# Kernel optimization log

Hardware: AMD Instinct MI355X
Metric: run time of the kernel (lower is better)

Reference implementation:

```python
import jax, jax.numpy as jnp
import numpy as np

N_NODES = 50000
N_EDGES = 1000000
D = 66
NEG_SLOPE = 0.2
EPS_BN = 1e-5


def _glorot(key, shape):
    fan = sum(shape)
    lim = jnp.sqrt(6.0 / fan)
    return jax.random.uniform(key, shape, jnp.float32, -lim, lim)


def setup_inputs() -> dict:
    key = jax.random.key(0)
    ks = jax.random.split(key, 40)
    inp = {
        'h': jax.random.normal(ks[0], (N_NODES, D), jnp.float32),
        'edge_index': jax.random.randint(ks[1], (2, N_EDGES), 0, N_NODES, jnp.int32),
        'edge_weight': jax.random.uniform(ks[2], (N_EDGES, 1), jnp.float32),
        'bn_gamma': jnp.ones((D,), jnp.float32),
        'bn_beta': jnp.zeros((D,), jnp.float32),
    }
    i = 3
    for l in (1, 2, 3):
        inp[f'W{l}'] = _glorot(ks[i], (D, D)); i += 1
        inp[f'b{l}'] = jnp.zeros((D,), jnp.float32)
        inp[f'att_src{l}'] = _glorot(ks[i], (D,)); i += 1
        inp[f'att_dst{l}'] = _glorot(ks[i], (D,)); i += 1
        inp[f'We{l}'] = _glorot(ks[i], (1, D)); i += 1
        inp[f'att_e{l}'] = _glorot(ks[i], (D,)); i += 1
    dims = [(D, D), (D, D), (D, D), (D, D), (D, 22)]
    for l, (din, dout) in enumerate(dims, start=1):
        inp[f'fc{l}_w'] = _glorot(ks[i], (din, dout)); i += 1
        inp[f'fc{l}_b'] = jnp.zeros((dout,), jnp.float32)
    return inp


def _gat_conv(h, src, dst, edge_weight, W, b, att_src, att_dst, We, att_e):
    x = h @ W                                     # [N, D]
    a_src = x @ att_src                           # [N]
    a_dst = x @ att_dst                           # [N]
    a_e = (edge_weight @ We) @ att_e              # [E]
    alpha = a_src[src] + a_dst[dst] + a_e         # [E]
    alpha = jnp.where(alpha > 0, alpha, NEG_SLOPE * alpha)
    # scatter-softmax over destination nodes
    m = jax.ops.segment_max(alpha, dst, num_segments=N_NODES)
    m = jnp.where(jnp.isfinite(m), m, 0.0)
    ex = jnp.exp(alpha - m[dst])
    denom = jax.ops.segment_sum(ex, dst, num_segments=N_NODES)
    coef = ex / (denom[dst] + 1e-16)              # [E]
    out = jax.ops.segment_sum(coef[:, None] * x[src], dst, num_segments=N_NODES)
    return out + b


def reference(h, edge_index, edge_weight, bn_gamma, bn_beta,
              W1, b1, att_src1, att_dst1, We1, att_e1,
              W2, b2, att_src2, att_dst2, We2, att_e2,
              W3, b3, att_src3, att_dst3, We3, att_e3,
              fc1_w, fc1_b, fc2_w, fc2_b, fc3_w, fc3_b,
              fc4_w, fc4_b, fc5_w, fc5_b):
    src, dst = edge_index[0], edge_index[1]
    # BatchNorm1d (training-mode batch statistics, biased variance)
    mean = h.mean(0)
    var = ((h - mean) ** 2).mean(0)
    x = (h - mean) * jax.lax.rsqrt(var + EPS_BN) * bn_gamma + bn_beta
    x = jax.nn.relu(_gat_conv(x, src, dst, edge_weight, W1, b1, att_src1, att_dst1, We1, att_e1))
    x = jax.nn.relu(_gat_conv(x, src, dst, edge_weight, W2, b2, att_src2, att_dst2, We2, att_e2))
    x = jax.nn.relu(_gat_conv(x, src, dst, edge_weight, W3, b3, att_src3, att_dst3, We3, att_e3))
    x = jax.nn.relu(x @ fc1_w + fc1_b)
    x = jax.nn.relu(x @ fc2_w + fc2_b)
    x = jax.nn.relu(x @ fc3_w + fc3_b)
    x = jax.nn.relu(x @ fc4_w + fc4_b)
    return x @ fc5_w + fc5_b
```

## Files before the change

kernel.cpp:

```cpp
#include <hip/hip_runtime.h>
#include <math.h>

#define D 66
#define SP 68
#define NEG_SLOPE 0.2f
#define CAP 6144

typedef short s8v __attribute__((ext_vector_type(8)));
typedef float f4v __attribute__((ext_vector_type(4)));

__device__ __forceinline__ float lrelu(float a){ return a > 0.f ? a : NEG_SLOPE * a; }
__device__ __forceinline__ void fma4(float4& a, float s, const float4& w){
  a.x = fmaf(s, w.x, a.x); a.y = fmaf(s, w.y, a.y);
  a.z = fmaf(s, w.z, a.z); a.w = fmaf(s, w.w, a.w);
}
__device__ __forceinline__ unsigned short bf16r(float f){
  unsigned u = __float_as_uint(f);
  u += 0x7FFFu + ((u >> 16) & 1u);
  return (unsigned short)(u >> 16);
}
__device__ __forceinline__ float bf16f(unsigned short b){
  return __uint_as_float(((unsigned)b) << 16);
}
__device__ __forceinline__ void split8t(const float* p, s8v& a0, s8v& a1, s8v& a2){
  #pragma unroll
  for (int j = 0; j < 8; j++){
    float v = p[j];
    unsigned u0 = __float_as_uint(v) & 0xFFFF0000u;
    float r1 = v - __uint_as_float(u0);
    unsigned u1 = __float_as_uint(r1) & 0xFFFF0000u;
    float r2 = r1 - __uint_as_float(u1);
    unsigned u2 = __float_as_uint(r2);
    a0[j] = (short)(u0 >> 16);
    a1[j] = (short)(u1 >> 16);
    a2[j] = (short)(u2 >> 16);
  }
}
#define MM6(acc, a0, a1, a2, b0v, b1v, b2v)                                \
  acc = __builtin_amdgcn_mfma_f32_16x16x32_bf16(a0, b0v, acc, 0, 0, 0);    \
  acc = __builtin_amdgcn_mfma_f32_16x16x32_bf16(a1, b0v, acc, 0, 0, 0);    \
  acc = __builtin_amdgcn_mfma_f32_16x16x32_bf16(a0, b1v, acc, 0, 0, 0);    \
  acc = __builtin_amdgcn_mfma_f32_16x16x32_bf16(a2, b0v, acc, 0, 0, 0);    \
  acc = __builtin_amdgcn_mfma_f32_16x16x32_bf16(a1, b1v, acc, 0, 0, 0);    \
  acc = __builtin_amdgcn_mfma_f32_16x16x32_bf16(a0, b2v, acc, 0, 0, 0);

__global__ __launch_bounds__(256) void k_stats_hist(const float* __restrict__ h, const int* __restrict__ dst,
                                                    float* __restrict__ sums, int* __restrict__ bhist,
                                                    int n, int E){
  int t = threadIdx.x;
  if (blockIdx.x < 256){
    __shared__ float ls[2 * D];
    if (t < 2 * D) ls[t] = 0.f;
    __syncthreads();
    int rpb = (n + 255) / 256;
    int r0 = blockIdx.x * rpb;
    int r1 = min(n, r0 + rpb);
    if (t < 3 * D){
      int c = t % D, seg = t / D;
      float s1 = 0.f, s2 = 0.f;
      for (int r = r0 + seg; r < r1; r += 3){
        float v = h[(size_t)r * D + c];
        s1 += v; s2 += v * v;
      }
      atomicAdd(&ls[c], s1);
      atomicAdd(&ls[D + c], s2);
    }
    __syncthreads();
    if (t < 2 * D) atomicAdd(&sums[t], ls[t]);
  } else {
    __shared__ int hh[256];
    hh[t] = 0;
    __syncthreads();
    int stride = 256 * 256;
    for (int e = (blockIdx.x - 256) * 256 + t; e < E; e += stride)
      atomicAdd(&hh[dst[e] >> 8], 1);
    __syncthreads();
    if (hh[t]) atomicAdd(&bhist[t], hh[t]);
  }
}

struct PrepArgs {
  const float *sums, *gamma, *beta;
  const float *We[3], *ae[3];
  const float *gw[3];
  const float *fw[5], *fb[5];
  float *misc; short *W0, *W1, *W2; short *F0, *F1, *F2; float *bpack;
  int n;
};

__global__ __launch_bounds__(256) void k_prep(PrepArgs pa){
  int t = threadIdx.x;
  if (blockIdx.x == 0){
    if (t < D){
      float mean = pa.sums[t] / (float)pa.n;
      float var  = pa.sums[D + t] / (float)pa.n - mean * mean;
      float inv  = rsqrtf(var + 1e-5f);
      float sc = pa.gamma[t] * inv;
      pa.misc[t] = sc;
      pa.misc[D + t] = pa.beta[t] - mean * sc;
    } else if (t >= D && t < D + 3){
      int l = t - D;
      float c = 0.f;
      for (int d = 0; d < D; d++) c += pa.We[l][d] * pa.ae[l][d];
      pa.misc[2 * D + l] = c;
    }
  } else if (blockIdx.x <= 12){
    int tid = (blockIdx.x - 1) * 256 + t;
    if (tid >= 3 * 960) return;
    int L = tid & 63;
    int ct = (tid >> 6) % 15;
    int lay = tid / 960;
    const float* w = pa.gw[lay];
    int c = ct / 5, tt = ct % 5;
    int nn = tt * 16 + (L & 15);
    int kb = c * 32 + (L >> 4) * 8;
    #pragma unroll
    for (int j = 0; j < 8; j++){
      int k = kb + j;
      float v = (k < D && nn < D) ? w[k * D + nn] : 0.f;
      unsigned short b0 = bf16r(v);  float f0 = bf16f(b0);
      float r1 = v - f0;
      unsigned short b1 = bf16r(r1); float f1 = bf16f(b1);
      unsigned short b2 = bf16r(r1 - f1);
      pa.W0[tid * 8 + j] = (short)b0;
      pa.W1[tid * 8 + j] = (short)b1;
      pa.W2[tid * 8 + j] = (short)b2;
    }
  } else {
    int tid = (blockIdx.x - 13) * 256 + t;
    if (tid < 5 * 960){
      int L = tid & 63;
      int ct = (tid >> 6) % 15;
      int lay = tid / 960;
      const float* w = pa.fw[lay];
      int ncol = (lay == 4) ? 22 : D;
      int c = ct / 5, tt = ct % 5;
      int nn = tt * 16 + (L & 15);
      int kb = c * 32 + (L >> 4) * 8;
      #pragma unroll
      for (int j = 0; j < 8; j++){
        int k = kb + j;
        float v = (k < D && nn < ncol) ? w[k * ncol + nn] : 0.f;
        unsigned short b0 = bf16r(v);  float f0 = bf16f(b0);
        float r1 = v - f0;
        unsigned short b1 = bf16r(r1); float f1 = bf16f(b1);
        unsigned short b2 = bf16r(r1 - f1);
        pa.F0[tid * 8 + j] = (short)b0;
        pa.F1[tid * 8 + j] = (short)b1;
        pa.F2[tid * 8 + j] = (short)b2;
      }
    } else if (tid < 5 * 960 + 400){
      int i = tid - 5 * 960;
      int lay = i / 80, col = i % 80;
      int ncol = (lay == 4) ? 22 : D;
      pa.bpack[i] = (col < ncol) ? pa.fb[lay][col] : 0.f;
    }
  }
}

__global__ void k_bscan(const int* __restrict__ bhist, int* __restrict__ bbase,
                        int* __restrict__ gcur, int* __restrict__ rowptr, int N, int E){
  __shared__ int sh[256];
  int t = threadIdx.x;
  int v = bhist[t];
  sh[t] = v; __syncthreads();
  for (int o = 1; o < 256; o <<= 1){
    int u = (t >= o) ? sh[t - o] : 0;
    __syncthreads();
    sh[t] += u;
    __syncthreads();
  }
  int ex = sh[t] - v;
  bbase[t] = ex;
  gcur[t] = ex;
  if (t == 255){ bbase[256] = sh[255]; rowptr[N] = E; }
}

#define PCHUNK 4096
__global__ __launch_bounds__(256) void k_part(const int* __restrict__ src, const int* __restrict__ dst,
                                              const float* __restrict__ ew,
                                              int* __restrict__ gcur, int2* __restrict__ tmp, int E){
  __shared__ int hist[256];
  __shared__ int base[256];
  int t = threadIdx.x;
  int e0 = blockIdx.x * PCHUNK;
  int eend = min(E, e0 + PCHUNK);
  hist[t] = 0;
  __syncthreads();
  for (int e = e0 + t; e < eend; e += 256)
    atomicAdd(&hist[dst[e] >> 8], 1);
  __syncthreads();
  if (hist[t] > 0) base[t] = atomicAdd(&gcur[t], hist[t]);
  hist[t] = 0;
  __syncthreads();
  for (int e = e0 + t; e < eend; e += 256){
    int d = dst[e];
    int b = d >> 8;
    int off = atomicAdd(&hist[b], 1);
    tmp[base[b] + off] = make_int2((src[e] & 0xffff) | ((d & 255) << 16), __float_as_int(ew[e]));
  }
}

__global__ __launch_bounds__(256) void k_bsort(const int2* __restrict__ tmp, const int* __restrict__ bbase,
                                               int2* __restrict__ epair, int* __restrict__ rowptr, int N){
  __shared__ int2 ebuf[CAP];
  __shared__ int lcnt[256];
  __shared__ int sc[256];
  __shared__ int lcur[256];
  int b = blockIdx.x, t = threadIdx.x;
  int s0 = bbase[b], s1 = bbase[b + 1];
  int cnt = s1 - s0;
  lcnt[t] = 0;
  __syncthreads();
  for (int j = t; j < cnt; j += 256){
    int2 e = tmp[s0 + j];
    if (j < CAP) ebuf[j] = e;
    atomicAdd(&lcnt[(e.x >> 16) & 255], 1);
  }
  __syncthreads();
  int v = lcnt[t];
  sc[t] = v; __syncthreads();
  for (int o = 1; o < 256; o <<= 1){
    int u = (t >= o) ? sc[t - o] : 0;
    __syncthreads();
    sc[t] += u;
    __syncthreads();
  }
  int ex = sc[t] - v;
  int node = (b << 8) + t;
  if (node < N) rowptr[node] = s0 + ex;
  lcur[t] = ex;
  __syncthreads();
  for (int j = t; j < cnt; j += 256){
    int2 e = (j < CAP) ? ebuf[j] : tmp[s0 + j];
    int i = (e.x >> 16) & 255;
    int p = atomicAdd(&lcur[i], 1);
    epair[s0 + p] = make_int2(e.x & 0xffff, e.y);
  }
}

template<bool BN_IN>
__global__ __launch_bounds__(256) void k_mm(const float* __restrict__ X,
    const short* __restrict__ W0, const short* __restrict__ W1, const short* __restrict__ W2,
    const float* __restrict__ att_s, const float* __restrict__ att_d,
    const float* __restrict__ bn,
    float* __restrict__ Y, float* __restrict__ a_src, float* __restrict__ a_dst, int n){
  const int wv = threadIdx.x >> 6, L = threadIdx.x & 63;
  const int quad = L >> 4, m = L & 15;
  const int row0 = blockIdx.x * 64 + wv * 16;
  const int lrow = min(row0 + m, n - 1);
  f4v acc[5];
  #pragma unroll
  for (int t = 0; t < 5; t++) acc[t] = (f4v){0.f,0.f,0.f,0.f};

  #pragma unroll
  for (int c = 0; c < 3; c++){
    float xv[8];
    if (c < 2){
      if (BN_IN){
        const float* hr = X + (size_t)lrow * D + c * 32 + quad * 8;
        #pragma unroll
        for (int j = 0; j < 8; j += 2){
          float2 hv = *(const float2*)(hr + j);
          int col = c * 32 + quad * 8 + j;
          xv[j]     = hv.x * bn[col]     + bn[D + col];
          xv[j + 1] = hv.y * bn[col + 1] + bn[D + col + 1];
        }
      } else {
        const float* xr = X + (size_t)lrow * SP;
        float4 p0 = *(const float4*)&xr[c * 32 + quad * 8];
        float4 p1 = *(const float4*)&xr[c * 32 + quad * 8 + 4];
        xv[0] = p0.x; xv[1] = p0.y; xv[2] = p0.z; xv[3] = p0.w;
        xv[4] = p1.x; xv[5] = p1.y; xv[6] = p1.z; xv[7] = p1.w;
      }
    } else {
      #pragma unroll
      for (int j = 0; j < 8; j++) xv[j] = 0.f;
      if (quad == 0){
        if (BN_IN){
          float2 hv = *(const float2*)(X + (size_t)lrow * D + 64);
          xv[0] = hv.x * bn[64] + bn[D + 64];
          xv[1] = hv.y * bn[65] + bn[D + 65];
        } else {
          float4 p0 = *(const float4*)&X[(size_t)lrow * SP + 64];
          xv[0] = p0.x; xv[1] = p0.y; xv[2] = p0.z; xv[3] = p0.w;
        }
      }
    }
    s8v a0, a1, a2;
    split8t(xv, a0, a1, a2);
    const short* b0p = W0 + (c * 5) * 512 + L * 8;
    const short* b1p = W1 + (c * 5) * 512 + L * 8;
    const short* b2p = W2 + (c * 5) * 512 + L * 8;
    #pragma unroll
    for (int t = 0; t < 5; t++){
      s8v b0v = *(const s8v*)(b0p + t * 512);
      s8v b1v = *(const s8v*)(b1p + t * 512);
      s8v b2v = *(const s8v*)(b2p + t * 512);
      MM6(acc[t], a0, a1, a2, b0v, b1v, b2v)
    }
  }

  float ps[4] = {0.f,0.f,0.f,0.f}, pd[4] = {0.f,0.f,0.f,0.f};
  #pragma unroll
  for (int t = 0; t < 5; t++){
    int col = t * 16 + m;
    float as_v = 0.f, ad_v = 0.f;
    if (col < D){ as_v = att_s[col]; ad_v = att_d[col]; }
    #pragma unroll
    for (int r = 0; r < 4; r++){
      ps[r] += acc[t][r] * as_v;
      pd[r] += acc[t][r] * ad_v;
    }
  }
  #pragma unroll
  for (int r = 0; r < 4; r++){
    int rw = row0 + quad * 4 + r;
    if (rw < n){
      float* yr = Y + (size_t)rw * SP;
      #pragma unroll
      for (int t = 0; t < 4; t++) yr[t * 16 + m] = acc[t][r];
      if (m < 4) yr[64 + m] = (m < 2) ? acc[4][r] : 0.f;
    }
  }
  #pragma unroll
  for (int o = 1; o <= 8; o <<= 1){
    #pragma unroll
    for (int r = 0; r < 4; r++){
      ps[r] += __shfl_xor(ps[r], o);
      pd[r] += __shfl_xor(pd[r], o);
    }
  }
  if (m == 0){
    #pragma unroll
    for (int r = 0; r < 4; r++){
      int rw = row0 + quad * 4 + r;
      if (rw < n){ a_src[rw] = ps[r]; a_dst[rw] = pd[r]; }
    }
  }
}

#define FST 84
__global__ __launch_bounds__(256) void k_fcmm(const float* __restrict__ X,
    const short* __restrict__ W0, const short* __restrict__ W1, const short* __restrict__ W2,
    const float* __restrict__ bpack, float* __restrict__ out, int n){
  __shared__ __align__(16) float xs[4][16][FST];
  const int wv = threadIdx.x >> 6, L = threadIdx.x & 63;
  const int quad = L >> 4, m = L & 15;
  const int row0 = blockIdx.x * 64 + wv * 16;
  const int lrow = min(row0 + m, n - 1);
  const float* xr = X + (size_t)lrow * SP;

  for (int l = 0; l < 5; l++){
    const int NTl = (l == 4) ? 2 : 5;
    f4v acc[5];
    #pragma unroll
    for (int t = 0; t < 5; t++) acc[t] = (f4v){0.f,0.f,0.f,0.f};
    #pragma unroll
    for (int c = 0; c < 3; c++){
      float xv[8];
      if (l == 0){
        if (c < 2){
          float4 p0 = *(const float4*)&xr[c * 32 + quad * 8];
          float4 p1 = *(const float4*)&xr[c * 32 + quad * 8 + 4];
          xv[0] = p0.x; xv[1] = p0.y; xv[2] = p0.z; xv[3] = p0.w;
          xv[4] = p1.x; xv[5] = p1.y; xv[6] = p1.z; xv[7] = p1.w;
        } else {
          float4 p0 = make_float4(0.f, 0.f, 0.f, 0.f);
          if (quad == 0) p0 = *(const float4*)&xr[64];
          xv[0] = p0.x; xv[1] = p0.y; xv[2] = p0.z; xv[3] = p0.w;
          xv[4] = 0.f; xv[5] = 0.f; xv[6] = 0.f; xv[7] = 0.f;
        }
      } else {
        if (c == 2 && quad >= 2){
          #pragma unroll
          for (int j = 0; j < 8; j++) xv[j] = 0.f;
        } else {
          float4 p0 = *(const float4*)&xs[wv][m][c * 32 + quad * 8];
          float4 p1 = *(const float4*)&xs[wv][m][c * 32 + quad * 8 + 4];
          xv[0] = p0.x; xv[1] = p0.y; xv[2] = p0.z; xv[3] = p0.w;
          xv[4] = p1.x; xv[5] = p1.y; xv[6] = p1.z; xv[7] = p1.w;
        }
      }
      s8v a0, a1, a2;
      split8t(xv, a0, a1, a2);
      const short* b0p = W0 + ((l * 3 + c) * 5) * 512 + L * 8;
      const short* b1p = W1 + ((l * 3 + c) * 5) * 512 + L * 8;
      const short* b2p = W2 + ((l * 3 + c) * 5) * 512 + L * 8;
      for (int t = 0; t < NTl; t++){
        s8v b0v = *(const s8v*)(b0p + t * 512);
        s8v b1v = *(const s8v*)(b1p + t * 512);
        s8v b2v = *(const s8v*)(b2p + t * 512);
        MM6(acc[t], a0, a1, a2, b0v, b1v, b2v)
      }
    }
    if (l < 4){
      #pragma unroll
      for (int t = 0; t < 5; t++){
        int col = t * 16 + m;
        float bv = bpack[l * 80 + col];
        #pragma unroll
        for (int r = 0; r < 4; r++){
          float v = acc[t][r] + bv;
          xs[wv][quad * 4 + r][col] = v > 0.f ? v : 0.f;
        }
      }
      __asm__ volatile("" ::: "memory");
    } else {
      #pragma unroll
      for (int t = 0; t < 2; t++){
        int col = t * 16 + m;
        #pragma unroll
        for (int r = 0; r < 4; r++){
          int rw = row0 + quad * 4 + r;
          if (col < 22 && rw < n) out[(size_t)rw * 22 + col] = acc[t][r] + bpack[4 * 80 + col];
        }
      }
    }
  }
}

__global__ __launch_bounds__(256) void k_agg(const float* __restrict__ y,
                                             const float* __restrict__ a_src, const float* __restrict__ a_dst,
                                             const int* __restrict__ rowptr, const int2* __restrict__ epair,
                                             const float* __restrict__ misc, int cidx,
                                             const float* __restrict__ bias,
                                             float* __restrict__ xout, int n){
  const int wid  = (int)((blockIdx.x * (size_t)blockDim.x + threadIdx.x) >> 6);
  const int lane = threadIdx.x & 63;
  if (wid >= n) return;
  const int beg = rowptr[wid];
  const int deg = rowptr[wid + 1] - beg;
  const float ce  = misc[2 * D + cidx];
  const float adn = a_dst[wid];
  const int g = lane >> 3, q = lane & 7;

  float4 accA = make_float4(0.f,0.f,0.f,0.f);
  float4 accB = make_float4(0.f,0.f,0.f,0.f);
  float2 tacc = make_float2(0.f,0.f);

  if (deg <= 64){
    int s = 0; float al = -INFINITY;
    bool act = lane < deg;
    if (act){
      int2 ep = epair[beg + lane];
      s = ep.x;
      al = lrelu(a_src[s] + adn + ce * __int_as_float(ep.y));
    }
    float mx = al;
    #pragma unroll
    for (int o = 32; o; o >>= 1) mx = fmaxf(mx, __shfl_xor(mx, o));
    float ex = act ? __expf(al - mx) : 0.f;
    float sum = ex;
    #pragma unroll
    for (int o = 32; o; o >>= 1) sum += __shfl_xor(sum, o);
    float coef = ex * (1.f / (sum + 1e-16f));
    for (int e0 = 0; e0 < deg; e0 += 8){
      int e = e0 + g;
      int   st = __shfl(s, e);
      float ct = __shfl(coef, e);
      if (e < deg){
        const float* row = y + (size_t)st * SP;
        float4 y0 = *(const float4*)&row[4 * q];
        float4 y1 = *(const float4*)&row[32 + 4 * q];
        fma4(accA, ct, y0);
        fma4(accB, ct, y1);
        if (q == 0){
          float2 tv = *(const float2*)&row[64];
          tacc.x += ct * tv.x; tacc.y += ct * tv.y;
        }
      }
    }
  } else {
    float mx = -INFINITY;
    for (int j0 = 0; j0 < deg; j0 += 64){
      int j = j0 + lane;
      if (j < deg){
        int2 ep = epair[beg + j];
        mx = fmaxf(mx, lrelu(a_src[ep.x] + adn + ce * __int_as_float(ep.y)));
      }
    }
    #pragma unroll
    for (int o = 32; o; o >>= 1) mx = fmaxf(mx, __shfl_xor(mx, o));
    float sum = 0.f;
    for (int j0 = 0; j0 < deg; j0 += 64){
      int j = j0 + lane;
      if (j < deg){
        int2 ep = epair[beg + j];
        sum += __expf(lrelu(a_src[ep.x] + adn + ce * __int_as_float(ep.y)) - mx);
      }
    }
    #pragma unroll
    for (int o = 32; o; o >>= 1) sum += __shfl_xor(sum, o);
    float inv = 1.f / (sum + 1e-16f);
    for (int j0 = 0; j0 < deg; j0 += 64){
      int cnt = min(64, deg - j0);
      int s = 0; float ex = 0.f;
      if (lane < cnt){
        int2 ep = epair[beg + j0 + lane];
        s = ep.x;
        ex = __expf(lrelu(a_src[s] + adn + ce * __int_as_float(ep.y)) - mx);
      }
      float coef = ex * inv;
      for (int e0 = 0; e0 < cnt; e0 += 8){
        int e = e0 + g;
        int   st = __shfl(s, e);
        float ct = __shfl(coef, e);
        if (e < cnt){
          const float* row = y + (size_t)st * SP;
          float4 y0 = *(const float4*)&row[4 * q];
          float4 y1 = *(const float4*)&row[32 + 4 * q];
          fma4(accA, ct, y0);
          fma4(accB, ct, y1);
          if (q == 0){
            float2 tv = *(const float2*)&row[64];
            tacc.x += ct * tv.x; tacc.y += ct * tv.y;
          }
        }
      }
    }
  }

  #pragma unroll
  for (int o = 8; o <= 32; o <<= 1){
    accA.x += __shfl_xor(accA.x, o); accA.y += __shfl_xor(accA.y, o);
    accA.z += __shfl_xor(accA.z, o); accA.w += __shfl_xor(accA.w, o);
    accB.x += __shfl_xor(accB.x, o); accB.y += __shfl_xor(accB.y, o);
    accB.z += __shfl_xor(accB.z, o); accB.w += __shfl_xor(accB.w, o);
    tacc.x += __shfl_xor(tacc.x, o); tacc.y += __shfl_xor(tacc.y, o);
  }
  float* orow = xout + (size_t)wid * SP;
  if (lane < 8){
    float4 v;
    v.x = accA.x + bias[4*lane+0]; v.x = v.x > 0.f ? v.x : 0.f;
    v.y = accA.y + bias[4*lane+1]; v.y = v.y > 0.f ? v.y : 0.f;
    v.z = accA.z + bias[4*lane+2]; v.z = v.z > 0.f ? v.z : 0.f;
    v.w = accA.w + bias[4*lane+3]; v.w = v.w > 0.f ? v.w : 0.f;
    *(float4*)&orow[4 * lane] = v;
  } else if (lane < 16){
    int qq = lane - 8;
    float4 v;
    v.x = accB.x + bias[32+4*qq+0]; v.x = v.x > 0.f ? v.x : 0.f;
    v.y = accB.y + bias[32+4*qq+1]; v.y = v.y > 0.f ? v.y : 0.f;
    v.z = accB.z + bias[32+4*qq+2]; v.z = v.z > 0.f ? v.z : 0.f;
    v.w = accB.w + bias[32+4*qq+3]; v.w = v.w > 0.f ? v.w : 0.f;
    *(float4*)&orow[32 + 4 * qq] = v;
  }
  if (lane == 0){
    float4 tv;
    tv.x = tacc.x + bias[64]; tv.x = tv.x > 0.f ? tv.x : 0.f;
    tv.y = tacc.y + bias[65]; tv.y = tv.y > 0.f ? tv.y : 0.f;
    tv.z = 0.f; tv.w = 0.f;
    *(float4*)&orow[64] = tv;
  }
}

extern "C" void kernel_launch(void* const* d_in, const int* in_sizes, int n_in,
                              void* d_out, int out_size, void* d_ws, size_t ws_size,
                              hipStream_t stream){
  const float* h     = (const float*)d_in[0];
  const int*   ei    = (const int*)  d_in[1];
  const float* ew    = (const float*)d_in[2];
  const float* gamma = (const float*)d_in[3];
  const float* beta  = (const float*)d_in[4];
  const float *Wl[3], *bl[3], *asl[3], *adl[3], *Wel[3], *ael[3];
  int idx = 5;
  for (int l = 0; l < 3; l++){
    Wl[l]  = (const float*)d_in[idx++];
    bl[l]  = (const float*)d_in[idx++];
    asl[l] = (const float*)d_in[idx++];
    adl[l] = (const float*)d_in[idx++];
    Wel[l] = (const float*)d_in[idx++];
    ael[l] = (const float*)d_in[idx++];
  }
  const float *fw[5], *fb[5];
  for (int l = 0; l < 5; l++){ fw[l] = (const float*)d_in[idx++]; fb[l] = (const float*)d_in[idx++]; }

  int N = in_sizes[0] / D;
  int E = in_sizes[1] / 2;
  const int* src  = ei;
  const int* dstp = ei + E;

  char* base = (char*)d_ws;
  size_t o = 0;
  auto alloc = [&](size_t b){ size_t r = o; o += (b + 255) & ~(size_t)255; return r; };
  float*  bufA   = (float*)(base + alloc((size_t)N * SP * 4));
  float*  bufB   = (float*)(base + alloc((size_t)N * SP * 4));
  float*  a_src  = (float*)(base + alloc((size_t)N * 4));
  float*  a_dst  = (float*)(base + alloc((size_t)N * 4));
  float*  misc   = (float*)(base + alloc(512 * 4));
  float*  sums   = (float*)(base + alloc(2 * D * 4));
  int*    rowptr = (int*)  (base + alloc((size_t)(N + 1) * 4));
  int*    bhist  = (int*)  (base + alloc(256 * 4));
  int*    bbase  = (int*)  (base + alloc(257 * 4));
  int*    gcur   = (int*)  (base + alloc(256 * 4));
  int2*   epair  = (int2*) (base + alloc((size_t)E * 8));
  short*  W0p    = (short*)(base + alloc(3 * 7680 * 2));
  short*  W1p    = (short*)(base + alloc(3 * 7680 * 2));
  short*  W2p    = (short*)(base + alloc(3 * 7680 * 2));
  short*  FW0p   = (short*)(base + alloc(5 * 7680 * 2));
  short*  FW1p   = (short*)(base + alloc(5 * 7680 * 2));
  short*  FW2p   = (short*)(base + alloc(5 * 7680 * 2));
  float*  bpack  = (float*)(base + alloc(400 * 4));
  int2*   tmp    = (int2*)bufB;

  hipMemsetAsync(sums, 0, 2 * D * 4, stream);
  hipMemsetAsync(bhist, 0, 256 * 4, stream);

  k_stats_hist<<<512, 256, 0, stream>>>(h, dstp, sums, bhist, N, E);

  PrepArgs pa;
  pa.sums = sums; pa.gamma = gamma; pa.beta = beta;
  for (int l = 0; l < 3; l++){ pa.We[l] = Wel[l]; pa.ae[l] = ael[l]; pa.gw[l] = Wl[l]; }
  for (int l = 0; l < 5; l++){ pa.fw[l] = fw[l]; pa.fb[l] = fb[l]; }
  pa.misc = misc; pa.W0 = W0p; pa.W1 = W1p; pa.W2 = W2p;
  pa.F0 = FW0p; pa.F1 = FW1p; pa.F2 = FW2p; pa.bpack = bpack; pa.n = N;
  k_prep<<<34, 256, 0, stream>>>(pa);

  int NB = (N + 255) >> 8;
  k_bscan<<<1, 256, 0, stream>>>(bhist, bbase, gcur, rowptr, N, E);
  k_part<<<(E + PCHUNK - 1) / PCHUNK, 256, 0, stream>>>(src, dstp, ew, gcur, tmp, E);
  k_bsort<<<NB, 256, 0, stream>>>(tmp, bbase, epair, rowptr, N);

  int gb = (N + 63) / 64;
  int ab = (N + 3) / 4;

  k_mm<true ><<<gb, 256, 0, stream>>>(h,    W0p + 0 * 7680, W1p + 0 * 7680, W2p + 0 * 7680,
                                      asl[0], adl[0], misc, bufB, a_src, a_dst, N);
  k_agg<<<ab, 256, 0, stream>>>(bufB, a_src, a_dst, rowptr, epair, misc, 0, bl[0], bufA, N);
  k_mm<false><<<gb, 256, 0, stream>>>(bufA, W0p + 1 * 7680, W1p + 1 * 7680, W2p + 1 * 7680,
                                      asl[1], adl[1], misc, bufB, a_src, a_dst, N);
  k_agg<<<ab, 256, 0, stream>>>(bufB, a_src, a_dst, rowptr, epair, misc, 1, bl[1], bufA, N);
  k_mm<false><<<gb, 256, 0, stream>>>(bufA, W0p + 2 * 7680, W1p + 2 * 7680, W2p + 2 * 7680,
                                      asl[2], adl[2], misc, bufB, a_src, a_dst, N);
  k_agg<<<ab, 256, 0, stream>>>(bufB, a_src, a_dst, rowptr, epair, misc, 2, bl[2], bufA, N);

  k_fcmm<<<gb, 256, 0, stream>>>(bufA, FW0p, FW1p, FW2p, bpack, (float*)d_out, N);
}
```

Measured before the change: 445.5 us.

## Split FC tiles across wave pairs and recompute softmax coefs per edge in aggregation

The FC-stack kernel now gives each 16-row group to two waves that split the output column tiles (3+2, or 1+1 for the last layer). Each block covers 32 rows instead of 64 and uses __syncthreads in place of per-wave barriers, which doubles the block count and shortens each wave's serial MFMA chain. The aggregation kernel drops the shuffle-based coefficient broadcast. Each 4-lane group now handles one edge and rereads its epair entry and a_src value to recompute exp, so 16 edges are processed per iteration, at the cost of redundant exp and gathers plus wider shuffle reductions.

```diff
diff --git a/kernel.cpp b/kernel.cpp
--- a/kernel.cpp
+++ b/kernel.cpp
@@ -344,18 +344,20 @@
 __global__ __launch_bounds__(256) void k_fcmm(const float* __restrict__ X,
     const short* __restrict__ W0, const short* __restrict__ W1, const short* __restrict__ W2,
     const float* __restrict__ bpack, float* __restrict__ out, int n){
-  __shared__ __align__(16) float xs[4][16][FST];
+  __shared__ __align__(16) float xs[2][16][FST];
   const int wv = threadIdx.x >> 6, L = threadIdx.x & 63;
   const int quad = L >> 4, m = L & 15;
-  const int row0 = blockIdx.x * 64 + wv * 16;
+  const int rg = wv >> 1, th = wv & 1;
+  const int row0 = blockIdx.x * 32 + rg * 16;
   const int lrow = min(row0 + m, n - 1);
   const float* xr = X + (size_t)lrow * SP;
 
   for (int l = 0; l < 5; l++){
-    const int NTl = (l == 4) ? 2 : 5;
-    f4v acc[5];
-    #pragma unroll
-    for (int t = 0; t < 5; t++) acc[t] = (f4v){0.f,0.f,0.f,0.f};
+    const int t0 = (l == 4) ? th : (th ? 3 : 0);
+    const int nt = (l == 4) ? 1  : (th ? 2 : 3);
+    f4v acc[3];
+    #pragma unroll
+    for (int t = 0; t < 3; t++) acc[t] = (f4v){0.f,0.f,0.f,0.f};
     #pragma unroll
     for (int c = 0; c < 3; c++){
       float xv[8];
@@ -376,18 +378,18 @@
           #pragma unroll
           for (int j = 0; j < 8; j++) xv[j] = 0.f;
         } else {
-          float4 p0 = *(const float4*)&xs[wv][m][c * 32 + quad * 8];
-          float4 p1 = *(const float4*)&xs[wv][m][c * 32 + quad * 8 + 4];
+          float4 p0 = *(const float4*)&xs[rg][m][c * 32 + quad * 8];
+          float4 p1 = *(const float4*)&xs[rg][m][c * 32 + quad * 8 + 4];
           xv[0] = p0.x; xv[1] = p0.y; xv[2] = p0.z; xv[3] = p0.w;
           xv[4] = p1.x; xv[5] = p1.y; xv[6] = p1.z; xv[7] = p1.w;
         }
       }
       s8v a0, a1, a2;
       split8t(xv, a0, a1, a2);
-      const short* b0p = W0 + ((l * 3 + c) * 5) * 512 + L * 8;
-      const short* b1p = W1 + ((l * 3 + c) * 5) * 512 + L * 8;
-      const short* b2p = W2 + ((l * 3 + c) * 5) * 512 + L * 8;
-      for (int t = 0; t < NTl; t++){
+      const short* b0p = W0 + ((l * 3 + c) * 5 + t0) * 512 + L * 8;
+      const short* b1p = W1 + ((l * 3 + c) * 5 + t0) * 512 + L * 8;
+      const short* b2p = W2 + ((l * 3 + c) * 5 + t0) * 512 + L * 8;
+      for (int t = 0; t < nt; t++){
         s8v b0v = *(const s8v*)(b0p + t * 512);
         s8v b1v = *(const s8v*)(b1p + t * 512);
         s8v b2v = *(const s8v*)(b2p + t * 512);
@@ -395,26 +397,23 @@
       }
     }
     if (l < 4){
-      #pragma unroll
-      for (int t = 0; t < 5; t++){
-        int col = t * 16 + m;
+      __syncthreads();
+      for (int t = 0; t < nt; t++){
+        int col = (t0 + t) * 16 + m;
         float bv = bpack[l * 80 + col];
         #pragma unroll
         for (int r = 0; r < 4; r++){
           float v = acc[t][r] + bv;
-          xs[wv][quad * 4 + r][col] = v > 0.f ? v : 0.f;
+          xs[rg][quad * 4 + r][col] = v > 0.f ? v : 0.f;
         }
       }
-      __asm__ volatile("" ::: "memory");
+      __syncthreads();
     } else {
+      int col = t0 * 16 + m;
       #pragma unroll
-      for (int t = 0; t < 2; t++){
-        int col = t * 16 + m;
-        #pragma unroll
-        for (int r = 0; r < 4; r++){
-          int rw = row0 + quad * 4 + r;
-          if (col < 22 && rw < n) out[(size_t)rw * 22 + col] = acc[t][r] + bpack[4 * 80 + col];
-        }
+      for (int r = 0; r < 4; r++){
+        int rw = row0 + quad * 4 + r;
+        if (col < 22 && rw < n) out[(size_t)rw * 22 + col] = acc[0][r] + bpack[4 * 80 + col];
       }
     }
   }
@@ -433,46 +432,24 @@
   const int deg = rowptr[wid + 1] - beg;
   const float ce  = misc[2 * D + cidx];
   const float adn = a_dst[wid];
-  const int g = lane >> 3, q = lane & 7;
-
-  float4 accA = make_float4(0.f,0.f,0.f,0.f);
-  float4 accB = make_float4(0.f,0.f,0.f,0.f);
-  float2 tacc = make_float2(0.f,0.f);
-
+
+  float mx, inv;
   if (deg <= 64){
-    int s = 0; float al = -INFINITY;
-    bool act = lane < deg;
-    if (act){
+    float al = -INFINITY;
+    if (lane < deg){
       int2 ep = epair[beg + lane];
-      s = ep.x;
-      al = lrelu(a_src[s] + adn + ce * __int_as_float(ep.y));
-    }
-    float mx = al;
+      al = lrelu(a_src[ep.x] + adn + ce * __int_as_float(ep.y));
+    }
+    mx = al;
     #pragma unroll
     for (int o = 32; o; o >>= 1) mx = fmaxf(mx, __shfl_xor(mx, o));
-    float ex = act ? __expf(al - mx) : 0.f;
+    float ex = (lane < deg) ? __expf(al - mx) : 0.f;
     float sum = ex;
     #pragma unroll
     for (int o = 32; o; o >>= 1) sum += __shfl_xor(sum, o);
-    float coef = ex * (1.f / (sum + 1e-16f));
-    for (int e0 = 0; e0 < deg; e0 += 8){
-      int e = e0 + g;
-      int   st = __shfl(s, e);
-      float ct = __shfl(coef, e);
-      if (e < deg){
-        const float* row = y + (size_t)st * SP;
-        float4 y0 = *(const float4*)&row[4 * q];
-        float4 y1 = *(const float4*)&row[32 + 4 * q];
-        fma4(accA, ct, y0);
-        fma4(accB, ct, y1);
-        if (q == 0){
-          float2 tv = *(const float2*)&row[64];
-          tacc.x += ct * tv.x; tacc.y += ct * tv.y;
-        }
-      }
-    }
+    inv = 1.f / (sum + 1e-16f);
   } else {
-    float mx = -INFINITY;
+    mx = -INFINITY;
     for (int j0 = 0; j0 < deg; j0 += 64){
       int j = j0 + lane;
       if (j < deg){
@@ -492,59 +469,69 @@
     }
     #pragma unroll
     for (int o = 32; o; o >>= 1) sum += __shfl_xor(sum, o);
-    float inv = 1.f / (sum + 1e-16f);
-    for (int j0 = 0; j0 < deg; j0 += 64){
-      int cnt = min(64, deg - j0);
-      int s = 0; float ex = 0.f;
-      if (lane < cnt){
-        int2 ep = epair[beg + j0 + lane];
-        s = ep.x;
-        ex = __expf(lrelu(a_src[s] + adn + ce * __int_as_float(ep.y)) - mx);
-      }
-      float coef = ex * inv;
-      for (int e0 = 0; e0 < cnt; e0 += 8){
-        int e = e0 + g;
-        int   st = __shfl(s, e);
-        float ct = __shfl(coef, e);
-        if (e < cnt){
-          const float* row = y + (size_t)st * SP;
-          float4 y0 = *(const float4*)&row[4 * q];
-          float4 y1 = *(const float4*)&row[32 + 4 * q];
-          fma4(accA, ct, y0);
-          fma4(accB, ct, y1);
-          if (q == 0){
-            float2 tv = *(const float2*)&row[64];
-            tacc.x += ct * tv.x; tacc.y += ct * tv.y;
-          }
-        }
+    inv = 1.f / (sum + 1e-16f);
+  }
+
+  const int g = lane >> 2, q = lane & 3;
+  float4 acc0 = make_float4(0.f,0.f,0.f,0.f);
+  float4 acc1 = make_float4(0.f,0.f,0.f,0.f);
+  float4 acc2 = make_float4(0.f,0.f,0.f,0.f);
+  float4 acc3 = make_float4(0.f,0.f,0.f,0.f);
+  float2 tacc = make_float2(0.f,0.f);
+  for (int e0 = 0; e0 < deg; e0 += 16){
+    int e = e0 + g;
+    if (e < deg){
+      int2 ep = epair[beg + e];
+      float co = __expf(lrelu(a_src[ep.x] + adn + ce * __int_as_float(ep.y)) - mx) * inv;
+      const float* row = y + (size_t)ep.x * SP;
+      fma4(acc0, co, *(const float4*)&row[      4 * q]);
+      fma4(acc1, co, *(const float4*)&row[16 + 4 * q]);
+      fma4(acc2, co, *(const float4*)&row[32 + 4 * q]);
+      fma4(acc3, co, *(const float4*)&row[48 + 4 * q]);
+      if (q == 0){
+        float2 tv = *(const float2*)&row[64];
+        tacc.x += co * tv.x; tacc.y += co * tv.y;
       }
     }
   }
 
   #pragma unroll
-  for (int o = 8; o <= 32; o <<= 1){
-    accA.x += __shfl_xor(accA.x, o); accA.y += __shfl_xor(accA.y, o);
-    accA.z += __shfl_xor(accA.z, o); accA.w += __shfl_xor(accA.w, o);
-    accB.x += __shfl_xor(accB.x, o); accB.y += __shfl_xor(accB.y, o);
-    accB.z += __shfl_xor(accB.z, o); accB.w += __shfl_xor(accB.w, o);
+  for (int o = 4; o <= 32; o <<= 1){
+    acc0.x += __shfl_xor(acc0.x, o); acc0.y += __shfl_xor(acc0.y, o);
+    acc0.z += __shfl_xor(acc0.z, o); acc0.w += __shfl_xor(acc0.w, o);
+    acc1.x += __shfl_xor(acc1.x, o); acc1.y += __shfl_xor(acc1.y, o);
+    acc1.z += __shfl_xor(acc1.z, o); acc1.w += __shfl_xor(acc1.w, o);
+    acc2.x += __shfl_xor(acc2.x, o); acc2.y += __shfl_xor(acc2.y, o);
+    acc2.z += __shfl_xor(acc2.z, o); acc2.w += __shfl_xor(acc2.w, o);
+    acc3.x += __shfl_xor(acc3.x, o); acc3.y += __shfl_xor(acc3.y, o);
+    acc3.z += __shfl_xor(acc3.z, o); acc3.w += __shfl_xor(acc3.w, o);
     tacc.x += __shfl_xor(tacc.x, o); tacc.y += __shfl_xor(tacc.y, o);
   }
+
   float* orow = xout + (size_t)wid * SP;
-  if (lane < 8){
+  if (lane < 4){
+    int c0 = 4 * lane;
     float4 v;
-    v.x = accA.x + bias[4*lane+0]; v.x = v.x > 0.f ? v.x : 0.f;
-    v.y = accA.y + bias[4*lane+1]; v.y = v.y > 0.f ? v.y : 0.f;
-    v.z = accA.z + bias[4*lane+2]; v.z = v.z > 0.f ? v.z : 0.f;
-    v.w = accA.w + bias[4*lane+3]; v.w = v.w > 0.f ? v.w : 0.f;
-    *(float4*)&orow[4 * lane] = v;
-  } else if (lane < 16){
-    int qq = lane - 8;
-    float4 v;
-    v.x = accB.x + bias[32+4*qq+0]; v.x = v.x > 0.f ? v.x : 0.f;
-    v.y = accB.y + bias[32+4*qq+1]; v.y = v.y > 0.f ? v.y : 0.f;
-    v.z = accB.z + bias[32+4*qq+2]; v.z = v.z > 0.f ? v.z : 0.f;
-    v.w = accB.w + bias[32+4*qq+3]; v.w = v.w > 0.f ? v.w : 0.f;
-    *(float4*)&orow[32 + 4 * qq] = v;
+    v.x = acc0.x + bias[c0+0]; v.x = v.x > 0.f ? v.x : 0.f;
+    v.y = acc0.y + bias[c0+1]; v.y = v.y > 0.f ? v.y : 0.f;
+    v.z = acc0.z + bias[c0+2]; v.z = v.z > 0.f ? v.z : 0.f;
+    v.w = acc0.w + bias[c0+3]; v.w = v.w > 0.f ? v.w : 0.f;
+    *(float4*)&orow[c0] = v;
+    v.x = acc1.x + bias[16+c0+0]; v.x = v.x > 0.f ? v.x : 0.f;
+    v.y = acc1.y + bias[16+c0+1]; v.y = v.y > 0.f ? v.y : 0.f;
+    v.z = acc1.z + bias[16+c0+2]; v.z = v.z > 0.f ? v.z : 0.f;
+    v.w = acc1.w + bias[16+c0+3]; v.w = v.w > 0.f ? v.w : 0.f;
+    *(float4*)&orow[16 + c0] = v;
+    v.x = acc2.x + bias[32+c0+0]; v.x = v.x > 0.f ? v.x : 0.f;
+    v.y = acc2.y + bias[32+c0+1]; v.y = v.y > 0.f ? v.y : 0.f;
+    v.z = acc2.z + bias[32+c0+2]; v.z = v.z > 0.f ? v.z : 0.f;
+    v.w = acc2.w + bias[32+c0+3]; v.w = v.w > 0.f ? v.w : 0.f;
+    *(float4*)&orow[32 + c0] = v;
+    v.x = acc3.x + bias[48+c0+0]; v.x = v.x > 0.f ? v.x : 0.f;
+    v.y = acc3.y + bias[48+c0+1]; v.y = v.y > 0.f ? v.y : 0.f;
+    v.z = acc3.z + bias[48+c0+2]; v.z = v.z > 0.f ? v.z : 0.f;
+    v.w = acc3.w + bias[48+c0+3]; v.w = v.w > 0.f ? v.w : 0.f;
+    *(float4*)&orow[48 + c0] = v;
   }
   if (lane == 0){
     float4 tv;
@@ -635,5 +622,6 @@
                                       asl[2], adl[2], misc, bufB, a_src, a_dst, N);
   k_agg<<<ab, 256, 0, stream>>>(bufB, a_src, a_dst, rowptr, epair, misc, 2, bl[2], bufA, N);
 
-  k_fcmm<<<gb, 256, 0, stream>>>(bufA, FW0p, FW1p, FW2p, bpack, (float*)d_out, N);
-}
+  int gb2 = (N + 31) / 32;
+  k_fcmm<<<gb2, 256, 0, stream>>>(bufA, FW0p, FW1p, FW2p, bpack, (float*)d_out, N);
+}
```

Result: slower. 487.3 us (+9.4%).
